# Kernel optimization log

Hardware: AMD Instinct MI355X
Metric: run time of the kernel (lower is better)

Reference implementation:

```python
import jax, jax.numpy as jnp
import numpy as np
import math

B, T, C, H = 2, 4096, 512, 8
HD = C // H


def setup_inputs() -> dict:
    key = jax.random.key(0)
    k1, k2, k3 = jax.random.split(key, 3)
    x = jax.random.normal(k1, (B, T, C), dtype=jnp.float32)
    # weights stored as [in, out] so y = x @ W (equivalent to torch Linear with W^T)
    w_qkv = jax.random.normal(k2, (C, 3 * C), dtype=jnp.float32) * (1.0 / math.sqrt(C))
    w_out = jax.random.normal(k3, (C, C), dtype=jnp.float32) * (1.0 / math.sqrt(C))
    return {"x": x, "w_qkv": w_qkv, "w_out": w_out}


def reference(x, w_qkv, w_out):
    Bs, Ts, Cs = x.shape
    qkv = x @ w_qkv                                   # [B,T,3C]
    q, k, v = jnp.split(qkv, 3, axis=-1)
    # [B,H,T,HD]
    q = q.reshape(Bs, Ts, H, HD).transpose(0, 2, 1, 3)
    k = k.reshape(Bs, Ts, H, HD).transpose(0, 2, 1, 3)
    v = v.reshape(Bs, Ts, H, HD).transpose(0, 2, 1, 3)
    scores = jnp.einsum("bhqd,bhkd->bhqk", q, k) / math.sqrt(HD)
    causal = jnp.tril(jnp.ones((Ts, Ts), dtype=bool))
    scores = jnp.where(causal[None, None], scores, -jnp.inf)
    attn = jax.nn.softmax(scores, axis=-1)            # [B,H,T,T]
    out = jnp.einsum("bhqk,bhkd->bhqd", attn, v)      # [B,H,T,HD]
    out = out.transpose(0, 2, 1, 3).reshape(Bs, Ts, Cs)
    return out @ w_out
```

## Files before the change

### kernel.cpp

```cpp
#include <hip/hip_runtime.h>
#include <hip/hip_bf16.h>

typedef __bf16 bf16;
typedef __bf16 bf16x4 __attribute__((ext_vector_type(4)));
typedef __bf16 bf16x8 __attribute__((ext_vector_type(8)));
typedef float f32x4 __attribute__((ext_vector_type(4)));

#define BB 2
#define TT 4096
#define CC 512
#define HH 8
#define HD 64
#define BHD 16
#define M_TOT 8192

#define SCL (0.125f * 1.44269504f)

#if __has_builtin(__builtin_amdgcn_exp2f)
#define EXP2F(x) __builtin_amdgcn_exp2f(x)
#else
#define EXP2F(x) exp2f(x)
#endif

#define GLDS(gptr, lptr)                                                     \
  __builtin_amdgcn_global_load_lds(                                          \
      (const __attribute__((address_space(1))) void*)(gptr),                 \
      (__attribute__((address_space(3))) void*)(lptr), 16, 0, 0)

__global__ __launch_bounds__(256) void convert_x_kernel(
    const float* __restrict__ X, bf16* __restrict__ Xb) {
  const size_t i0 = ((size_t)blockIdx.x * 256 + threadIdx.x) * 16;
  const float4* p = (const float4*)(X + i0);
#pragma unroll
  for (int c = 0; c < 2; ++c) {
    float4 a = p[c * 2], b = p[c * 2 + 1];
    bf16x8 v;
    v[0] = (bf16)a.x; v[1] = (bf16)a.y; v[2] = (bf16)a.z; v[3] = (bf16)a.w;
    v[4] = (bf16)b.x; v[5] = (bf16)b.y; v[6] = (bf16)b.z; v[7] = (bf16)b.w;
    *(bf16x8*)&Xb[i0 + c * 8] = v;
  }
}

__global__ __launch_bounds__(256) void transpose_w_kernel(
    const float* __restrict__ Wq, const float* __restrict__ Wo,
    bf16* __restrict__ WQT, bf16* __restrict__ WOT) {
  __shared__ float tile[64][65];
  int b = blockIdx.x;
  const float* W; bf16* WT; int N, n0, k0;
  if (b < 192) { W = Wq; WT = WQT; N = 1536; n0 = (b % 24) * 64; k0 = (b / 24) * 64; }
  else { b -= 192; W = Wo; WT = WOT; N = 512; n0 = (b & 7) * 64; k0 = (b >> 3) * 64; }
  const int t = threadIdx.x;
  const int rr = t >> 4, cc4 = (t & 15) * 4;
#pragma unroll
  for (int i = 0; i < 4; ++i) {
    float4 v = *(const float4*)&W[(size_t)(k0 + rr + i * 16) * N + n0 + cc4];
    tile[rr + i * 16][cc4 + 0] = v.x;
    tile[rr + i * 16][cc4 + 1] = v.y;
    tile[rr + i * 16][cc4 + 2] = v.z;
    tile[rr + i * 16][cc4 + 3] = v.w;
  }
  __syncthreads();
#pragma unroll
  for (int i = 0; i < 4; ++i) {
    const int nn = rr + i * 16;
    bf16x4 o;
#pragma unroll
    for (int j = 0; j < 4; ++j) o[j] = (bf16)tile[cc4 + j][nn];
    *(bf16x4*)&WT[(size_t)(n0 + nn) * 512 + k0 + cc4] = o;
  }
}

__global__ __launch_bounds__(256) void gemm_qkv_kernel(
    const bf16* __restrict__ Xb, const bf16* __restrict__ Wt,
    bf16* __restrict__ qw, bf16* __restrict__ kw, bf16* __restrict__ vw) {
  __shared__ __align__(16) bf16 As[128 * 64];
  __shared__ __align__(16) bf16 Bs[128 * 64];
  const int tid = threadIdx.x;
  const int wid = tid >> 6, lane = tid & 63, ln = lane & 15, hi = lane >> 4;
  const int wr = wid >> 1, wc = wid & 1;
  const int m0 = blockIdx.x * 128, n0 = blockIdx.y * 128;
  const int srow = lane >> 3, srcc = (lane & 7) ^ srow;

  f32x4 acc[4][4] = {};

  for (int k0 = 0; k0 < 512; k0 += 64) {
    __syncthreads();
#pragma unroll
    for (int i = 0; i < 4; ++i) {
      const int rb = 32 * wid + 8 * i;
      GLDS(&Xb[(size_t)(m0 + rb + srow) * 512 + k0 + srcc * 8], &As[rb * 64]);
      GLDS(&Wt[(size_t)(n0 + rb + srow) * 512 + k0 + srcc * 8], &Bs[rb * 64]);
    }
    __syncthreads();

    bf16x8 af[4][2], bfr[4][2];
#pragma unroll
    for (int mi = 0; mi < 4; ++mi) {
      const int row = wr * 64 + mi * 16 + ln, rs = row & 7;
      af[mi][0] = *(const bf16x8*)&As[row * 64 + ((hi ^ rs) * 8)];
      af[mi][1] = *(const bf16x8*)&As[row * 64 + (((4 + hi) ^ rs) * 8)];
    }
#pragma unroll
    for (int ni = 0; ni < 4; ++ni) {
      const int row = wc * 64 + ni * 16 + ln, rs = row & 7;
      bfr[ni][0] = *(const bf16x8*)&Bs[row * 64 + ((hi ^ rs) * 8)];
      bfr[ni][1] = *(const bf16x8*)&Bs[row * 64 + (((4 + hi) ^ rs) * 8)];
    }
#pragma unroll
    for (int mi = 0; mi < 4; ++mi)
#pragma unroll
      for (int ni = 0; ni < 4; ++ni) {
        acc[mi][ni] = __builtin_amdgcn_mfma_f32_16x16x32_bf16(af[mi][0], bfr[ni][0], acc[mi][ni], 0, 0, 0);
        acc[mi][ni] = __builtin_amdgcn_mfma_f32_16x16x32_bf16(af[mi][1], bfr[ni][1], acc[mi][ni], 0, 0, 0);
      }
  }

#pragma unroll
  for (int mi = 0; mi < 4; ++mi) {
    int rowb = m0 + wr * 64 + mi * 16 + hi * 4;
    int b = rowb >> 12, t0 = rowb & 4095;
#pragma unroll
    for (int ni = 0; ni < 4; ++ni) {
      int n = n0 + wc * 64 + ni * 16 + ln;
      int which = n >> 9, c = n & 511, h = c >> 6, d = c & 63;
      if (which == 2) {
        bf16x4 pv;
#pragma unroll
        for (int r = 0; r < 4; ++r) pv[r] = (bf16)acc[mi][ni][r];
        *(bf16x4*)&vw[((size_t)(b * HH + h) * HD + d) * TT + t0] = pv;
      } else {
        bf16* dst = which ? kw : qw;
        const float sc = which ? 1.0f : SCL;
#pragma unroll
        for (int r = 0; r < 4; ++r)
          dst[((size_t)(b * HH + h) * TT + t0 + r) * HD + d] = (bf16)(acc[mi][ni][r] * sc);
      }
    }
  }
}

__global__ __launch_bounds__(256) void attn_piece_kernel(
    const bf16* __restrict__ qw, const bf16* __restrict__ kw,
    const bf16* __restrict__ vt,
    bf16* __restrict__ po, float* __restrict__ pl) {
  __shared__ __align__(16) bf16 Ks[2][64 * 64];
  __shared__ __align__(16) bf16 Vs[2][64 * 64];
  const int tid = threadIdx.x;
  const int wid = tid >> 6, lane = tid & 63, ln = lane & 15, hi = lane >> 4;

  int qb, bh, chunk;
  {
    const int pid = blockIdx.x;
    if (pid < 1024)      { qb = 63 - (pid >> 6); int r = pid & 63;  bh = r >> 2; chunk = r & 3; }
    else if (pid < 1792) { int l = pid - 1024; qb = 47 - l / 48; int r = l % 48; bh = r / 3; chunk = r % 3; }
    else if (pid < 2304) { int l = pid - 1792; qb = 31 - (l >> 5); int r = l & 31; bh = r >> 1; chunk = r & 1; }
    else                 { int l = pid - 2304; qb = 15 - (l >> 4); bh = l & 15; chunk = 0; }
  }
  const int t0 = chunk * 16;
  const int t1 = (t0 + 16 < qb + 1) ? (t0 + 16) : (qb + 1);
  const int pid = blockIdx.x;

  const int q0w = qb * 64 + wid * 16;

  const int lrow8 = lane >> 3, lch = lane & 7;
  const int srcch = lch ^ lrow8;
  const int rbase = 8 * wid + lrow8;
  const size_t kb = (size_t)bh * TT * HD, vb = (size_t)bh * HD * TT;

  bf16x8 qf[2];
#pragma unroll
  for (int h = 0; h < 2; ++h)
    qf[h] = *(const bf16x8*)&qw[((size_t)bh * TT + q0w + ln) * HD + h * 32 + hi * 8];

  const bf16* kp[4][2];
#pragma unroll
  for (int kt = 0; kt < 4; ++kt) {
    const int krow = kt * 16 + ln;
    kp[kt][0] = &Ks[0][krow * 64 + ((hi ^ (ln & 7)) * 8)];
    kp[kt][1] = &Ks[0][krow * 64 + (((4 + hi) ^ (ln & 7)) * 8)];
  }
  const bf16* vp[4][2][2];
#pragma unroll
  for (int db = 0; db < 4; ++db) {
    const int d = db * 16 + ln, rowb = d * 64, dx = d & 7;
#pragma unroll
    for (int h2 = 0; h2 < 2; ++h2) {
      const int c1 = h2 * 4 + (hi >> 1);
      vp[db][h2][0] = &Vs[0][rowb + ((c1 ^ dx) * 8) + (hi & 1) * 4];
      vp[db][h2][1] = &Vs[0][rowb + (((c1 + 2) ^ dx) * 8) + (hi & 1) * 4];
    }
  }

  f32x4 o[4] = {};
  f32x4 osum = {};

  bf16x8 vones;
#pragma unroll
  for (int j = 0; j < 8; ++j) vones[j] = (bf16)1.0f;

  {
    const int kv = t0 * 64;
    GLDS(kw + kb + (size_t)(kv + rbase) * HD + srcch * 8, &Ks[0][(8 * wid) * 64]);
    GLDS(kw + kb + (size_t)(kv + 32 + rbase) * HD + srcch * 8, &Ks[0][(32 + 8 * wid) * 64]);
    GLDS(vt + vb + (size_t)rbase * TT + kv + srcch * 8, &Vs[0][(8 * wid) * 64]);
    GLDS(vt + vb + (size_t)(32 + rbase) * TT + kv + srcch * 8, &Vs[0][(32 + 8 * wid) * 64]);
  }
  const bf16* pk0 = kw + kb + (size_t)((t0 + 1) * 64 + rbase) * HD + srcch * 8;
  const bf16* pk1 = pk0 + (size_t)32 * HD;
  const bf16* pv0 = vt + vb + (size_t)rbase * TT + (t0 + 1) * 64 + srcch * 8;
  const bf16* pv1 = pv0 + (size_t)32 * TT;
  __syncthreads();

#define TILE(t_, BUF) do {                                                   \
    const int kv0 = (t_) * 64;                                               \
    if ((t_) + 1 < t1) {                                                     \
      GLDS(pk0, &Ks[(BUF) ^ 1][(8 * wid) * 64]);                             \
      GLDS(pk1, &Ks[(BUF) ^ 1][(32 + 8 * wid) * 64]);                        \
      GLDS(pv0, &Vs[(BUF) ^ 1][(8 * wid) * 64]);                             \
      GLDS(pv1, &Vs[(BUF) ^ 1][(32 + 8 * wid) * 64]);                        \
      pk0 += (size_t)64 * HD; pk1 += (size_t)64 * HD; pv0 += 64; pv1 += 64;  \
    }                                                                        \
    f32x4 s[4];                                                              \
    __builtin_amdgcn_s_setprio(1);                                           \
    _Pragma("unroll")                                                        \
    for (int kt = 0; kt < 4; ++kt) {                                         \
      bf16x8 kf0 = *(const bf16x8*)(kp[kt][0] + (BUF) * 4096);               \
      bf16x8 kf1 = *(const bf16x8*)(kp[kt][1] + (BUF) * 4096);               \
      f32x4 a = {};                                                          \
      a = __builtin_amdgcn_mfma_f32_16x16x32_bf16(kf0, qf[0], a, 0, 0, 0);   \
      a = __builtin_amdgcn_mfma_f32_16x16x32_bf16(kf1, qf[1], a, 0, 0, 0);   \
      s[kt] = a;                                                             \
    }                                                                        \
    __builtin_amdgcn_s_setprio(0);                                           \
    if ((t_) == qb) {                                                        \
      const int qg = q0w + ln;                                               \
      _Pragma("unroll")                                                      \
      for (int kt = 0; kt < 4; ++kt)                                         \
        _Pragma("unroll")                                                    \
        for (int r = 0; r < 4; ++r)                                          \
          if (kv0 + kt * 16 + hi * 4 + r > qg) s[kt][r] = -1e30f;            \
    }                                                                        \
    _Pragma("unroll")                                                        \
    for (int kt = 0; kt < 4; ++kt)                                           \
      _Pragma("unroll")                                                      \
      for (int r = 0; r < 4; ++r) s[kt][r] = EXP2F(s[kt][r]);                \
    bf16x8 pa[2];                                                            \
    _Pragma("unroll")                                                        \
    for (int h2 = 0; h2 < 2; ++h2)                                           \
      _Pragma("unroll")                                                      \
      for (int j = 0; j < 8; ++j)                                            \
        pa[h2][j] = (bf16)s[h2 * 2 + (j >> 2)][j & 3];                       \
    __builtin_amdgcn_s_setprio(1);                                           \
    osum = __builtin_amdgcn_mfma_f32_16x16x32_bf16(pa[0], vones, osum, 0, 0, 0); \
    osum = __builtin_amdgcn_mfma_f32_16x16x32_bf16(pa[1], vones, osum, 0, 0, 0); \
    _Pragma("unroll")                                                        \
    for (int db = 0; db < 4; ++db) {                                         \
      _Pragma("unroll")                                                      \
      for (int h2 = 0; h2 < 2; ++h2) {                                       \
        bf16x4 lo = *(const bf16x4*)(vp[db][h2][0] + (BUF) * 4096);          \
        bf16x4 hi4 = *(const bf16x4*)(vp[db][h2][1] + (BUF) * 4096);         \
        bf16x8 vf = __builtin_shufflevector(lo, hi4, 0, 1, 2, 3, 4, 5, 6, 7); \
        o[db] = __builtin_amdgcn_mfma_f32_16x16x32_bf16(pa[h2], vf, o[db], 0, 0, 0); \
      }                                                                      \
    }                                                                        \
    __builtin_amdgcn_s_setprio(0);                                           \
    __syncthreads();                                                         \
  } while (0)

  int t = t0;
  for (; t + 1 < t1; t += 2) { TILE(t, 0); TILE(t + 1, 1); }
  if (t < t1) TILE(t, 0);

  {
    bf16* ob = po + (size_t)pid * 4096;
#pragma unroll
    for (int db = 0; db < 4; ++db)
#pragma unroll
      for (int r = 0; r < 4; ++r)
        ob[(wid * 16 + hi * 4 + r) * 64 + db * 16 + ln] = (bf16)o[db][r];
    if (ln == 0) {
#pragma unroll
      for (int r = 0; r < 4; ++r)
        pl[pid * 64 + wid * 16 + hi * 4 + r] = osum[r];
    }
  }
#undef TILE
}

__global__ __launch_bounds__(256) void attn_combine_kernel(
    const bf16* __restrict__ po, const float* __restrict__ pl,
    bf16* __restrict__ aw) {
  const int cb = blockIdx.x;
  const int qb = 63 - (cb >> 4), bh = cb & 15;
  const int tid = threadIdx.x;
  const int q_ = tid >> 2, dc = (tid & 3) * 16;

  const int nch = (qb >> 4) + 1;
  const int base = (qb >= 48) ? 0 : (qb >= 32) ? 1024 : (qb >= 16) ? 1792 : 2304;
  const int top  = (qb >= 48) ? 63 : (qb >= 32) ? 47 : (qb >= 16) ? 31 : 15;
  const int p0 = base + (top - qb) * 16 * nch + bh * nch;

  float sum = 0.f;
  for (int c = 0; c < nch; ++c) sum += pl[(p0 + c) * 64 + q_];
  const float inv = 1.0f / sum;

  float acc[16] = {};
  for (int c = 0; c < nch; ++c) {
    const bf16* ob = po + (size_t)(p0 + c) * 4096 + q_ * 64 + dc;
#pragma unroll
    for (int cc = 0; cc < 2; ++cc) {
      bf16x8 x = *(const bf16x8*)&ob[cc * 8];
#pragma unroll
      for (int j = 0; j < 8; ++j) acc[cc * 8 + j] += (float)x[j];
    }
  }
  bf16* dst = aw + ((size_t)bh * TT + qb * 64 + q_) * 64 + dc;
#pragma unroll
  for (int cc = 0; cc < 2; ++cc) {
    bf16x8 outv;
#pragma unroll
    for (int j = 0; j < 8; ++j) outv[j] = (bf16)(acc[cc * 8 + j] * inv);
    *(bf16x8*)&dst[cc * 8] = outv;
  }
}

__global__ __launch_bounds__(256) void gemm_out_kernel(
    const bf16* __restrict__ A, const bf16* __restrict__ Wot,
    float* __restrict__ out) {
  __shared__ __align__(16) bf16 As[128 * 64];
  __shared__ __align__(16) bf16 Bs[64 * 64];
  const int tid = threadIdx.x;
  const int wid = tid >> 6, lane = tid & 63, ln = lane & 15, hi = lane >> 4;
  const int wr = wid >> 1, wc = wid & 1;
  const int m0 = blockIdx.x * 128, n0 = blockIdx.y * 64;
  const int srow = lane >> 3, srcc = (lane & 7) ^ srow;

  f32x4 acc[4][2] = {};

  for (int k0 = 0; k0 < 512; k0 += 64) {
    const int h = k0 >> 6;
    __syncthreads();
#pragma unroll
    for (int i = 0; i < 4; ++i) {
      const int rb = 32 * wid + 8 * i;
      const int m = m0 + rb + srow;
      const int b = m >> 12, t = m & 4095;
      GLDS(&A[((size_t)(b * HH + h) * TT + t) * HD + srcc * 8], &As[rb * 64]);
    }
#pragma unroll
    for (int i = 0; i < 2; ++i) {
      const int rb = 16 * wid + 8 * i;
      GLDS(&Wot[(size_t)(n0 + rb + srow) * 512 + k0 + srcc * 8], &Bs[rb * 64]);
    }
    __syncthreads();

    bf16x8 af[4][2], bfr[2][2];
#pragma unroll
    for (int mi = 0; mi < 4; ++mi) {
      const int row = wr * 64 + mi * 16 + ln, rs = row & 7;
      af[mi][0] = *(const bf16x8*)&As[row * 64 + ((hi ^ rs) * 8)];
      af[mi][1] = *(const bf16x8*)&As[row * 64 + (((4 + hi) ^ rs) * 8)];
    }
#pragma unroll
    for (int ni = 0; ni < 2; ++ni) {
      const int row = wc * 32 + ni * 16 + ln, rs = row & 7;
      bfr[ni][0] = *(const bf16x8*)&Bs[row * 64 + ((hi ^ rs) * 8)];
      bfr[ni][1] = *(const bf16x8*)&Bs[row * 64 + (((4 + hi) ^ rs) * 8)];
    }
#pragma unroll
    for (int mi = 0; mi < 4; ++mi)
#pragma unroll
      for (int ni = 0; ni < 2; ++ni) {
        acc[mi][ni] = __builtin_amdgcn_mfma_f32_16x16x32_bf16(af[mi][0], bfr[ni][0], acc[mi][ni], 0, 0, 0);
        acc[mi][ni] = __builtin_amdgcn_mfma_f32_16x16x32_bf16(af[mi][1], bfr[ni][1], acc[mi][ni], 0, 0, 0);
      }
  }

#pragma unroll
  for (int mi = 0; mi < 4; ++mi) {
    int rowb = m0 + wr * 64 + mi * 16 + hi * 4;
#pragma unroll
    for (int ni = 0; ni < 2; ++ni) {
      int n = n0 + wc * 32 + ni * 16 + ln;
#pragma unroll
      for (int r = 0; r < 4; ++r)
        out[(size_t)(rowb + r) * 512 + n] = acc[mi][ni][r];
    }
  }
}

extern "C" void kernel_launch(void* const* d_in, const int* in_sizes, int n_in,
                              void* d_out, int out_size, void* d_ws, size_t ws_size,
                              hipStream_t stream) {
  const float* x = (const float*)d_in[0];
  const float* w_qkv = (const float*)d_in[1];
  const float* w_out = (const float*)d_in[2];
  float* out = (float*)d_out;

  const size_t QKV_ELEMS = (size_t)BHD * TT * HD;
  bf16* qw = (bf16*)d_ws;
  bf16* kw = qw + QKV_ELEMS;
  bf16* vw = kw + QKV_ELEMS;
  bf16* aw = vw + QKV_ELEMS;
  bf16* po = aw + QKV_ELEMS;
  float* pl = (float*)(po + (size_t)2560 * 4096);
  bf16* wqt = (bf16*)(pl + (size_t)2560 * 64);
  bf16* wot = wqt + (size_t)1536 * 512;
  bf16* xb = po;

  convert_x_kernel<<<1024, 256, 0, stream>>>(x, xb);
  transpose_w_kernel<<<256, 256, 0, stream>>>(w_qkv, w_out, wqt, wot);
  gemm_qkv_kernel<<<dim3(M_TOT / 128, 1536 / 128), 256, 0, stream>>>(xb, wqt, qw, kw, vw);
  attn_piece_kernel<<<2560, 256, 0, stream>>>(qw, kw, vw, po, pl);
  attn_combine_kernel<<<1024, 256, 0, stream>>>(po, pl, aw);
  gemm_out_kernel<<<dim3(M_TOT / 128, 512 / 64), 256, 0, stream>>>(aw, wot, out);
}
```

Baseline: 115.5 us.

## Enlarge attention query tile to 128 rows per block, two 16-row subtiles per wave

Each attention block now covers 128 query rows instead of 64, with every wave computing two 16-row query subtiles that share each K/V fragment loaded from LDS. This halves the number of blocks and the K/V global-to-LDS traffic per query, and tiles that are fully masked for a wave are skipped. The partial buffers and the combine kernel are re-indexed to match. The cost is more registers per wave, fewer blocks for load balancing, and idle waves on the diagonal tiles.

```diff
diff --git a/kernel.cpp b/kernel.cpp
--- a/kernel.cpp
+++ b/kernel.cpp
@@ -151,26 +151,29 @@
   int qb, bh, chunk;
   {
     const int pid = blockIdx.x;
-    if (pid < 1024)      { qb = 63 - (pid >> 6); int r = pid & 63;  bh = r >> 2; chunk = r & 3; }
-    else if (pid < 1792) { int l = pid - 1024; qb = 47 - l / 48; int r = l % 48; bh = r / 3; chunk = r % 3; }
-    else if (pid < 2304) { int l = pid - 1792; qb = 31 - (l >> 5); int r = l & 31; bh = r >> 1; chunk = r & 1; }
-    else                 { int l = pid - 2304; qb = 15 - (l >> 4); bh = l & 15; chunk = 0; }
-  }
-  const int t0 = chunk * 16;
-  const int t1 = (t0 + 16 < qb + 1) ? (t0 + 16) : (qb + 1);
+    if (pid < 512)       { qb = 31 - (pid >> 6); int r = pid & 63; bh = r >> 2; chunk = r & 3; }
+    else if (pid < 896)  { int l = pid - 512; qb = 23 - l / 48; int r = l % 48; bh = r / 3; chunk = r % 3; }
+    else if (pid < 1152) { int l = pid - 896; qb = 15 - (l >> 5); int r = l & 31; bh = r >> 1; chunk = r & 1; }
+    else                 { int l = pid - 1152; qb = 7 - (l >> 4); bh = l & 15; chunk = 0; }
+  }
+  const int t0c = chunk * 16;
+  const int ntot = 2 * qb + 2;
+  const int t1 = (t0c + 16 < ntot) ? (t0c + 16) : ntot;
   const int pid = blockIdx.x;
 
-  const int q0w = qb * 64 + wid * 16;
+  const int q0w = qb * 128 + wid * 32;
 
   const int lrow8 = lane >> 3, lch = lane & 7;
   const int srcch = lch ^ lrow8;
   const int rbase = 8 * wid + lrow8;
   const size_t kb = (size_t)bh * TT * HD, vb = (size_t)bh * HD * TT;
 
-  bf16x8 qf[2];
-#pragma unroll
-  for (int h = 0; h < 2; ++h)
-    qf[h] = *(const bf16x8*)&qw[((size_t)bh * TT + q0w + ln) * HD + h * 32 + hi * 8];
+  bf16x8 qf[2][2];
+#pragma unroll
+  for (int qi = 0; qi < 2; ++qi)
+#pragma unroll
+    for (int h = 0; h < 2; ++h)
+      qf[qi][h] = *(const bf16x8*)&qw[((size_t)bh * TT + q0w + qi * 16 + ln) * HD + h * 32 + hi * 8];
 
   const bf16* kp[4][2];
 #pragma unroll
@@ -191,23 +194,23 @@
     }
   }
 
-  f32x4 o[4] = {};
-  f32x4 osum = {};
+  f32x4 o[2][4] = {};
+  f32x4 osum[2] = {};
 
   bf16x8 vones;
 #pragma unroll
   for (int j = 0; j < 8; ++j) vones[j] = (bf16)1.0f;
 
   {
-    const int kv = t0 * 64;
+    const int kv = t0c * 64;
     GLDS(kw + kb + (size_t)(kv + rbase) * HD + srcch * 8, &Ks[0][(8 * wid) * 64]);
     GLDS(kw + kb + (size_t)(kv + 32 + rbase) * HD + srcch * 8, &Ks[0][(32 + 8 * wid) * 64]);
     GLDS(vt + vb + (size_t)rbase * TT + kv + srcch * 8, &Vs[0][(8 * wid) * 64]);
     GLDS(vt + vb + (size_t)(32 + rbase) * TT + kv + srcch * 8, &Vs[0][(32 + 8 * wid) * 64]);
   }
-  const bf16* pk0 = kw + kb + (size_t)((t0 + 1) * 64 + rbase) * HD + srcch * 8;
+  const bf16* pk0 = kw + kb + (size_t)((t0c + 1) * 64 + rbase) * HD + srcch * 8;
   const bf16* pk1 = pk0 + (size_t)32 * HD;
-  const bf16* pv0 = vt + vb + (size_t)rbase * TT + (t0 + 1) * 64 + srcch * 8;
+  const bf16* pv0 = vt + vb + (size_t)rbase * TT + (t0c + 1) * 64 + srcch * 8;
   const bf16* pv1 = pv0 + (size_t)32 * TT;
   __syncthreads();
 
@@ -220,68 +223,89 @@
       GLDS(pv1, &Vs[(BUF) ^ 1][(32 + 8 * wid) * 64]);                        \
       pk0 += (size_t)64 * HD; pk1 += (size_t)64 * HD; pv0 += 64; pv1 += 64;  \
     }                                                                        \
-    f32x4 s[4];                                                              \
-    __builtin_amdgcn_s_setprio(1);                                           \
-    _Pragma("unroll")                                                        \
-    for (int kt = 0; kt < 4; ++kt) {                                         \
-      bf16x8 kf0 = *(const bf16x8*)(kp[kt][0] + (BUF) * 4096);               \
-      bf16x8 kf1 = *(const bf16x8*)(kp[kt][1] + (BUF) * 4096);               \
-      f32x4 a = {};                                                          \
-      a = __builtin_amdgcn_mfma_f32_16x16x32_bf16(kf0, qf[0], a, 0, 0, 0);   \
-      a = __builtin_amdgcn_mfma_f32_16x16x32_bf16(kf1, qf[1], a, 0, 0, 0);   \
-      s[kt] = a;                                                             \
+    if (kv0 <= q0w + 31) {                                                   \
+      f32x4 s[2][4];                                                         \
+      __builtin_amdgcn_s_setprio(1);                                         \
+      _Pragma("unroll")                                                      \
+      for (int kt = 0; kt < 4; ++kt) {                                       \
+        bf16x8 kf0 = *(const bf16x8*)(kp[kt][0] + (BUF) * 4096);             \
+        bf16x8 kf1 = *(const bf16x8*)(kp[kt][1] + (BUF) * 4096);             \
+        _Pragma("unroll")                                                    \
+        for (int qi = 0; qi < 2; ++qi) {                                     \
+          f32x4 a = {};                                                      \
+          a = __builtin_amdgcn_mfma_f32_16x16x32_bf16(kf0, qf[qi][0], a, 0, 0, 0); \
+          a = __builtin_amdgcn_mfma_f32_16x16x32_bf16(kf1, qf[qi][1], a, 0, 0, 0); \
+          s[qi][kt] = a;                                                     \
+        }                                                                    \
+      }                                                                      \
+      __builtin_amdgcn_s_setprio(0);                                         \
+      _Pragma("unroll")                                                      \
+      for (int qi = 0; qi < 2; ++qi) {                                       \
+        if (kv0 + 63 > q0w + qi * 16) {                                      \
+          const int qg = q0w + qi * 16 + ln;                                 \
+          _Pragma("unroll")                                                  \
+          for (int kt = 0; kt < 4; ++kt)                                     \
+            _Pragma("unroll")                                                \
+            for (int r = 0; r < 4; ++r)                                      \
+              if (kv0 + kt * 16 + hi * 4 + r > qg) s[qi][kt][r] = -1e30f;    \
+        }                                                                    \
+      }                                                                      \
+      _Pragma("unroll")                                                      \
+      for (int qi = 0; qi < 2; ++qi)                                         \
+        _Pragma("unroll")                                                    \
+        for (int kt = 0; kt < 4; ++kt)                                       \
+          _Pragma("unroll")                                                  \
+          for (int r = 0; r < 4; ++r) s[qi][kt][r] = EXP2F(s[qi][kt][r]);    \
+      bf16x8 pa[2][2];                                                       \
+      _Pragma("unroll")                                                      \
+      for (int qi = 0; qi < 2; ++qi)                                         \
+        _Pragma("unroll")                                                    \
+        for (int h2 = 0; h2 < 2; ++h2)                                       \
+          _Pragma("unroll")                                                  \
+          for (int j = 0; j < 8; ++j)                                        \
+            pa[qi][h2][j] = (bf16)s[qi][h2 * 2 + (j >> 2)][j & 3];           \
+      __builtin_amdgcn_s_setprio(1);                                         \
+      _Pragma("unroll")                                                      \
+      for (int qi = 0; qi < 2; ++qi) {                                       \
+        osum[qi] = __builtin_amdgcn_mfma_f32_16x16x32_bf16(pa[qi][0], vones, osum[qi], 0, 0, 0); \
+        osum[qi] = __builtin_amdgcn_mfma_f32_16x16x32_bf16(pa[qi][1], vones, osum[qi], 0, 0, 0); \
+      }                                                                      \
+      _Pragma("unroll")                                                      \
+      for (int db = 0; db < 4; ++db) {                                       \
+        _Pragma("unroll")                                                    \
+        for (int h2 = 0; h2 < 2; ++h2) {                                     \
+          bf16x4 lo = *(const bf16x4*)(vp[db][h2][0] + (BUF) * 4096);        \
+          bf16x4 hi4 = *(const bf16x4*)(vp[db][h2][1] + (BUF) * 4096);       \
+          bf16x8 vf = __builtin_shufflevector(lo, hi4, 0, 1, 2, 3, 4, 5, 6, 7); \
+          _Pragma("unroll")                                                  \
+          for (int qi = 0; qi < 2; ++qi)                                     \
+            o[qi][db] = __builtin_amdgcn_mfma_f32_16x16x32_bf16(pa[qi][h2], vf, o[qi][db], 0, 0, 0); \
+        }                                                                    \
+      }                                                                      \
+      __builtin_amdgcn_s_setprio(0);                                         \
     }                                                                        \
-    __builtin_amdgcn_s_setprio(0);                                           \
-    if ((t_) == qb) {                                                        \
-      const int qg = q0w + ln;                                               \
-      _Pragma("unroll")                                                      \
-      for (int kt = 0; kt < 4; ++kt)                                         \
-        _Pragma("unroll")                                                    \
-        for (int r = 0; r < 4; ++r)                                          \
-          if (kv0 + kt * 16 + hi * 4 + r > qg) s[kt][r] = -1e30f;            \
-    }                                                                        \
-    _Pragma("unroll")                                                        \
-    for (int kt = 0; kt < 4; ++kt)                                           \
-      _Pragma("unroll")                                                      \
-      for (int r = 0; r < 4; ++r) s[kt][r] = EXP2F(s[kt][r]);                \
-    bf16x8 pa[2];                                                            \
-    _Pragma("unroll")                                                        \
-    for (int h2 = 0; h2 < 2; ++h2)                                           \
-      _Pragma("unroll")                                                      \
-      for (int j = 0; j < 8; ++j)                                            \
-        pa[h2][j] = (bf16)s[h2 * 2 + (j >> 2)][j & 3];                       \
-    __builtin_amdgcn_s_setprio(1);                                           \
-    osum = __builtin_amdgcn_mfma_f32_16x16x32_bf16(pa[0], vones, osum, 0, 0, 0); \
-    osum = __builtin_amdgcn_mfma_f32_16x16x32_bf16(pa[1], vones, osum, 0, 0, 0); \
-    _Pragma("unroll")                                                        \
-    for (int db = 0; db < 4; ++db) {                                         \
-      _Pragma("unroll")                                                      \
-      for (int h2 = 0; h2 < 2; ++h2) {                                       \
-        bf16x4 lo = *(const bf16x4*)(vp[db][h2][0] + (BUF) * 4096);          \
-        bf16x4 hi4 = *(const bf16x4*)(vp[db][h2][1] + (BUF) * 4096);         \
-        bf16x8 vf = __builtin_shufflevector(lo, hi4, 0, 1, 2, 3, 4, 5, 6, 7); \
-        o[db] = __builtin_amdgcn_mfma_f32_16x16x32_bf16(pa[h2], vf, o[db], 0, 0, 0); \
-      }                                                                      \
-    }                                                                        \
-    __builtin_amdgcn_s_setprio(0);                                           \
     __syncthreads();                                                         \
   } while (0)
 
-  int t = t0;
+  int t = t0c;
   for (; t + 1 < t1; t += 2) { TILE(t, 0); TILE(t + 1, 1); }
   if (t < t1) TILE(t, 0);
 
   {
-    bf16* ob = po + (size_t)pid * 4096;
-#pragma unroll
-    for (int db = 0; db < 4; ++db)
-#pragma unroll
-      for (int r = 0; r < 4; ++r)
-        ob[(wid * 16 + hi * 4 + r) * 64 + db * 16 + ln] = (bf16)o[db][r];
+    bf16* ob = po + (size_t)pid * 8192;
+#pragma unroll
+    for (int qi = 0; qi < 2; ++qi)
+#pragma unroll
+      for (int db = 0; db < 4; ++db)
+#pragma unroll
+        for (int r = 0; r < 4; ++r)
+          ob[(wid * 32 + qi * 16 + hi * 4 + r) * 64 + db * 16 + ln] = (bf16)o[qi][db][r];
     if (ln == 0) {
 #pragma unroll
-      for (int r = 0; r < 4; ++r)
-        pl[pid * 64 + wid * 16 + hi * 4 + r] = osum[r];
+      for (int qi = 0; qi < 2; ++qi)
+#pragma unroll
+        for (int r = 0; r < 4; ++r)
+          pl[pid * 128 + wid * 32 + qi * 16 + hi * 4 + r] = osum[qi][r];
     }
   }
 #undef TILE
@@ -291,32 +315,33 @@
     const bf16* __restrict__ po, const float* __restrict__ pl,
     bf16* __restrict__ aw) {
   const int cb = blockIdx.x;
-  const int qb = 63 - (cb >> 4), bh = cb & 15;
+  const int qb = 31 - (cb >> 4), bh = cb & 15;
   const int tid = threadIdx.x;
-  const int q_ = tid >> 2, dc = (tid & 3) * 16;
-
-  const int nch = (qb >> 4) + 1;
-  const int base = (qb >= 48) ? 0 : (qb >= 32) ? 1024 : (qb >= 16) ? 1792 : 2304;
-  const int top  = (qb >= 48) ? 63 : (qb >= 32) ? 47 : (qb >= 16) ? 31 : 15;
-  const int p0 = base + (top - qb) * 16 * nch + bh * nch;
+  const int q_ = tid >> 1, dc = (tid & 1) * 32;
+
+  int nch, p0;
+  if (qb >= 24)      { nch = 4; p0 = (31 - qb) * 64 + bh * 4; }
+  else if (qb >= 16) { nch = 3; p0 = 512 + (23 - qb) * 48 + bh * 3; }
+  else if (qb >= 8)  { nch = 2; p0 = 896 + (15 - qb) * 32 + bh * 2; }
+  else               { nch = 1; p0 = 1152 + (7 - qb) * 16 + bh; }
 
   float sum = 0.f;
-  for (int c = 0; c < nch; ++c) sum += pl[(p0 + c) * 64 + q_];
+  for (int c = 0; c < nch; ++c) sum += pl[(p0 + c) * 128 + q_];
   const float inv = 1.0f / sum;
 
-  float acc[16] = {};
+  float acc[32] = {};
   for (int c = 0; c < nch; ++c) {
-    const bf16* ob = po + (size_t)(p0 + c) * 4096 + q_ * 64 + dc;
-#pragma unroll
-    for (int cc = 0; cc < 2; ++cc) {
+    const bf16* ob = po + (size_t)(p0 + c) * 8192 + q_ * 64 + dc;
+#pragma unroll
+    for (int cc = 0; cc < 4; ++cc) {
       bf16x8 x = *(const bf16x8*)&ob[cc * 8];
 #pragma unroll
       for (int j = 0; j < 8; ++j) acc[cc * 8 + j] += (float)x[j];
     }
   }
-  bf16* dst = aw + ((size_t)bh * TT + qb * 64 + q_) * 64 + dc;
-#pragma unroll
-  for (int cc = 0; cc < 2; ++cc) {
+  bf16* dst = aw + ((size_t)bh * TT + qb * 128 + q_) * 64 + dc;
+#pragma unroll
+  for (int cc = 0; cc < 4; ++cc) {
     bf16x8 outv;
 #pragma unroll
     for (int j = 0; j < 8; ++j) outv[j] = (bf16)(acc[cc * 8 + j] * inv);
@@ -403,15 +428,15 @@
   bf16* vw = kw + QKV_ELEMS;
   bf16* aw = vw + QKV_ELEMS;
   bf16* po = aw + QKV_ELEMS;
-  float* pl = (float*)(po + (size_t)2560 * 4096);
-  bf16* wqt = (bf16*)(pl + (size_t)2560 * 64);
+  float* pl = (float*)(po + (size_t)1280 * 8192);
+  bf16* wqt = (bf16*)(pl + (size_t)1280 * 128);
   bf16* wot = wqt + (size_t)1536 * 512;
   bf16* xb = po;
 
   convert_x_kernel<<<1024, 256, 0, stream>>>(x, xb);
   transpose_w_kernel<<<256, 256, 0, stream>>>(w_qkv, w_out, wqt, wot);
   gemm_qkv_kernel<<<dim3(M_TOT / 128, 1536 / 128), 256, 0, stream>>>(xb, wqt, qw, kw, vw);
-  attn_piece_kernel<<<2560, 256, 0, stream>>>(qw, kw, vw, po, pl);
-  attn_combine_kernel<<<1024, 256, 0, stream>>>(po, pl, aw);
+  attn_piece_kernel<<<1280, 256, 0, stream>>>(qw, kw, vw, po, pl);
+  attn_combine_kernel<<<512, 256, 0, stream>>>(po, pl, aw);
   gemm_out_kernel<<<dim3(M_TOT / 128, 512 / 64), 256, 0, stream>>>(aw, wot, out);
 }
```

After: 121.8 us. 5.4% more time.
